# Performance work log

Hardware: AMD Instinct MI355X
Metric: run time of the kernel (lower is better)

Reference implementation:

```python
import jax, jax.numpy as jnp
import numpy as np

HIDDEN = 1024
HEADS = 16
HEAD_DIM = HIDDEN // HEADS


def rotate_half(x):
    x1, x2 = jnp.split(x, 2, axis=-1)
    return jnp.concatenate([-x2, x1], axis=-1)


def rope_cos_sin(T, head_dim):
    inv_freq = 1.0 / (10000.0 ** (jnp.arange(0, head_dim, 2, dtype=jnp.float32) / head_dim))
    pos = jnp.arange(T, dtype=jnp.float32)
    freqs = jnp.einsum('i,j->ij', pos, inv_freq)          # [T, head_dim/2]
    emb = jnp.concatenate([freqs, freqs], axis=-1)        # [T, head_dim]
    # broadcast shape [1, T, 1, head_dim]
    return jnp.cos(emb)[None, :, None, :], jnp.sin(emb)[None, :, None, :]


def setup_inputs() -> dict:
    key = jax.random.key(0)
    ks = jax.random.split(key, 9)
    B, T = 4, 2048
    s = 1.0 / np.sqrt(HIDDEN)
    x = jax.random.normal(ks[0], (B, T, HIDDEN), dtype=jnp.float32)
    Wq = jax.random.uniform(ks[1], (HIDDEN, HIDDEN), minval=-s, maxval=s, dtype=jnp.float32)
    bq = jax.random.uniform(ks[2], (HIDDEN,), minval=-s, maxval=s, dtype=jnp.float32)
    Wk = jax.random.uniform(ks[3], (HIDDEN, HIDDEN), minval=-s, maxval=s, dtype=jnp.float32)
    bk = jax.random.uniform(ks[4], (HIDDEN,), minval=-s, maxval=s, dtype=jnp.float32)
    Wv = jax.random.uniform(ks[5], (HIDDEN, HIDDEN), minval=-s, maxval=s, dtype=jnp.float32)
    bv = jax.random.uniform(ks[6], (HIDDEN,), minval=-s, maxval=s, dtype=jnp.float32)
    Wo = jax.random.uniform(ks[7], (HIDDEN, HIDDEN), minval=-s, maxval=s, dtype=jnp.float32)
    bo = jax.random.uniform(ks[8], (HIDDEN,), minval=-s, maxval=s, dtype=jnp.float32)
    return {"x": x, "Wq": Wq, "bq": bq, "Wk": Wk, "bk": bk,
            "Wv": Wv, "bv": bv, "Wo": Wo, "bo": bo}


def reference(x, Wq, bq, Wk, bk, Wv, bv, Wo, bo):
    B, T, _ = x.shape
    q = (x @ Wq + bq).reshape(B, T, HEADS, HEAD_DIM)
    k = (x @ Wk + bk).reshape(B, T, HEADS, HEAD_DIM)
    v = (x @ Wv + bv).reshape(B, T, HEADS, HEAD_DIM)
    cos, sin = rope_cos_sin(T, HEAD_DIM)
    q = q * cos + rotate_half(q) * sin
    k = k * cos + rotate_half(k) * sin
    scale = jnp.sqrt(jnp.float32(HEAD_DIM))
    scores = jnp.einsum('bqhd,bkhd->bhqk', q, k) / scale   # [B,H,T,T]
    causal = jnp.tril(jnp.ones((T, T), dtype=bool))
    scores = jnp.where(causal[None, None], scores, -jnp.inf)
    probs = jax.nn.softmax(scores, axis=-1)
    attn = jnp.einsum('bhqk,bkhd->bqhd', probs, v).reshape(B, T, HIDDEN)
    return attn @ Wo + bo
```

## Files before the change

### kernel.cpp

```cpp
#include <hip/hip_runtime.h>

typedef unsigned short u16;
typedef __attribute__((ext_vector_type(4))) float f32x4;
typedef __attribute__((ext_vector_type(16))) float f32x16;
typedef __attribute__((ext_vector_type(8))) short s16x8;

#define B_   4
#define T_   2048
#define H_   16
#define D_   64
#define HID  1024
#define BT   (B_*T_)
#define N3   3072

#define BARRIER() do { asm volatile("" ::: "memory"); __builtin_amdgcn_s_barrier(); asm volatile("" ::: "memory"); } while (0)

__device__ inline u16 f2b(float f) {
  union { float f; unsigned u; } v; v.f = f;
  unsigned u = v.u;
  unsigned r = (u + 0x7FFFu + ((u >> 16) & 1u)) >> 16;
  return (u16)r;
}

__device__ inline void gll16(const u16* g, u16* l) {
  __builtin_amdgcn_global_load_lds(
      (const __attribute__((address_space(1))) unsigned int*)g,
      (__attribute__((address_space(3))) unsigned int*)l, 16, 0, 0);
}

__device__ inline int swz8(int row) { return (row ^ (row >> 3)) & 7; }

__global__ void k_cast4(const float* __restrict__ src, u16* __restrict__ dst, int n4) {
  int i = blockIdx.x * blockDim.x + threadIdx.x;
  if (i >= n4) return;
  float4 v = ((const float4*)src)[i];
  ushort4 o;
  o.x = f2b(v.x); o.y = f2b(v.y); o.z = f2b(v.z); o.w = f2b(v.w);
  ((ushort4*)dst)[i] = o;
}

__global__ void k_ropetab(float2* __restrict__ tab) {
  int i = blockIdx.x * blockDim.x + threadIdx.x;
  int d = i & 31, t = i >> 5;
  float inv = expf(-0.28782313662425574f * (float)d);
  float ang = (float)t * inv;
  float c, s;
  sincosf(ang, &s, &c);
  tab[i] = make_float2(c, s);
}

__global__ __launch_bounds__(256) void k_packT(const float* __restrict__ W0,
                                               const float* __restrict__ W1,
                                               const float* __restrict__ W2,
                                               u16* __restrict__ Wt) {
  __shared__ float L[64][68];
  int n0 = blockIdx.x * 64, k0 = blockIdx.y * 64;
  int which = n0 >> 10;
  const float* W = (which == 0) ? W0 : (which == 1) ? W1 : W2;
  int nc = n0 & 1023;
  int tid = threadIdx.x;
  #pragma unroll
  for (int i = 0; i < 4; i++) {
    int ch = tid + 256 * i;
    int kr = ch >> 4, cc = ch & 15;
    float4 v = *(const float4*)(W + (size_t)(k0 + kr) * 1024 + nc + cc * 4);
    *(float4*)(&L[kr][cc * 4]) = v;
  }
  __syncthreads();
  #pragma unroll
  for (int i = 0; i < 2; i++) {
    int ch = tid + 256 * i;
    int nr = ch >> 3, ck = ch & 7;
    u16 tmp[8];
    #pragma unroll
    for (int j = 0; j < 8; j++) tmp[j] = f2b(L[ck * 8 + j][nr]);
    *(uint4*)(Wt + (size_t)(n0 + nr) * 1024 + k0 + ck * 8) = *(uint4*)tmp;
  }
}

__global__ __launch_bounds__(512) void gemm256(
    const u16* __restrict__ A, const u16* __restrict__ Bt,
    const float* __restrict__ b0, const float* __restrict__ b1,
    const float* __restrict__ b2, const float2* __restrict__ tab,
    u16* __restrict__ outp)
{
  __shared__ __align__(16) char SM[135168];
  const int tid = threadIdx.x, lane = tid & 63, w = tid >> 6;
  const int l15 = lane & 15, g = lane >> 4;
  const int wm = (w >> 2) * 128, wn = (w & 3) * 64;
  const int mbase = blockIdx.y * 256, nbase = blockIdx.x * 256;
  const int K = 1024, NT = 32;
  f32x4 acc[8][4] = {};

  auto SA = [&](int buf, int t) {
    u16* dst = (u16*)(SM + buf * 32768);
    #pragma unroll
    for (int i = 0; i < 2; i++) {
      int f = w * 128 + i * 64 + lane;
      int row = f >> 2, c = (f & 3) ^ (row & 3);
      gll16(A + (size_t)(mbase + row) * K + t * 32 + c * 8, dst + f * 8);
    }
  };
  auto SB = [&](int buf, int t) {
    u16* dst = (u16*)(SM + buf * 32768 + 16384);
    #pragma unroll
    for (int i = 0; i < 2; i++) {
      int f = w * 128 + i * 64 + lane;
      int row = f >> 2, c = (f & 3) ^ (row & 3);
      gll16(Bt + (size_t)(nbase + row) * K + t * 32 + c * 8, dst + f * 8);
    }
  };

  SA(0, 0); SB(0, 0); SA(1, 1); SB(1, 1);
  asm volatile("s_waitcnt vmcnt(4)" ::: "memory");
  BARRIER();

  int cur = 0;
  for (int t = 0; t < NT; t++) {
    int nx = cur + 2; if (nx >= 3) nx -= 3;
    const char* Ab = SM + cur * 32768;
    const char* Bb = SM + cur * 32768 + 16384;
    bool st = (t + 2 < NT);

    s16x8 af[8], bf[4];
    #pragma unroll
    for (int mt = 0; mt < 8; mt++) {
      int row = wm + mt * 16 + l15;
      af[mt] = *(const s16x8*)(Ab + row * 64 + (g ^ (row & 3)) * 16);
    }
    #pragma unroll
    for (int nt = 0; nt < 2; nt++) {
      int row = wn + nt * 16 + l15;
      bf[nt] = *(const s16x8*)(Bb + row * 64 + (g ^ (row & 3)) * 16);
    }
    if (st) SA(nx, t + 2);
    BARRIER();
    __builtin_amdgcn_s_setprio(1);
    #pragma unroll
    for (int mt = 0; mt < 8; mt++) {
      acc[mt][0] = __builtin_amdgcn_mfma_f32_16x16x32_bf16(af[mt], bf[0], acc[mt][0], 0, 0, 0);
      acc[mt][1] = __builtin_amdgcn_mfma_f32_16x16x32_bf16(af[mt], bf[1], acc[mt][1], 0, 0, 0);
    }
    __builtin_amdgcn_s_setprio(0);
    BARRIER();

    #pragma unroll
    for (int nt = 2; nt < 4; nt++) {
      int row = wn + nt * 16 + l15;
      bf[nt] = *(const s16x8*)(Bb + row * 64 + (g ^ (row & 3)) * 16);
    }
    if (st) SB(nx, t + 2);
    BARRIER();
    __builtin_amdgcn_s_setprio(1);
    #pragma unroll
    for (int mt = 0; mt < 8; mt++) {
      acc[mt][2] = __builtin_amdgcn_mfma_f32_16x16x32_bf16(af[mt], bf[2], acc[mt][2], 0, 0, 0);
      acc[mt][3] = __builtin_amdgcn_mfma_f32_16x16x32_bf16(af[mt], bf[3], acc[mt][3], 0, 0, 0);
    }
    __builtin_amdgcn_s_setprio(0);
    if (t + 1 < NT) {
      if (st) asm volatile("s_waitcnt vmcnt(4)" ::: "memory");
      else    asm volatile("s_waitcnt vmcnt(0)" ::: "memory");
    }
    BARRIER();
    cur = (cur == 2) ? 0 : cur + 1;
  }

  int which = nbase >> 10;
  const float* bp = (which == 0) ? b0 : (which == 1) ? b1 : b2;
  u16* Lt = (u16*)SM;
  if (which < 2) {
    const float FSC = (which == 0) ? 0.18033688011112043f : 1.0f;
    #pragma unroll
    for (int mt = 0; mt < 8; mt++) {
      #pragma unroll
      for (int r = 0; r < 4; r++) {
        int ml = wm + mt * 16 + g * 4 + r;
        int t = (mbase + ml) & (T_ - 1);
        #pragma unroll
        for (int nt = 0; nt < 2; nt++) {
          int d = nt * 16 + l15;
          float2 cs = tab[t * 32 + d];
          float a0 = acc[mt][nt][r]     + bp[(nbase + wn + d) & 1023];
          float a1 = acc[mt][nt + 2][r] + bp[(nbase + wn + d + 32) & 1023];
          Lt[ml * 264 + wn + d]      = f2b((a0 * cs.x - a1 * cs.y) * FSC);
          Lt[ml * 264 + wn + d + 32] = f2b((a1 * cs.x + a0 * cs.y) * FSC);
        }
      }
    }
    __syncthreads();
    #pragma unroll
    for (int i = 0; i < 16; i++) {
      int c = tid + 512 * i;
      int row = c >> 5, cc = c & 31;
      int gm = mbase + row, t = gm & (T_ - 1), bb = gm >> 11;
      int gn0 = nbase + cc * 8, h = (gn0 >> 6) & 15, d0 = gn0 & 63;
      *(uint4*)(outp + ((size_t)((which * B_ + bb) * H_ + h) * T_ + t) * D_ + d0) =
          *(const uint4*)(Lt + row * 264 + cc * 8);
    }
  } else {
    #pragma unroll
    for (int mt = 0; mt < 8; mt++) {
      #pragma unroll
      for (int nt = 0; nt < 4; nt++) {
        int nl = wn + nt * 16 + l15;
        float bias = bp[(nbase + nl) & 1023];
        u16 t4[4];
        #pragma unroll
        for (int r = 0; r < 4; r++) t4[r] = f2b(acc[mt][nt][r] + bias);
        *(uint2*)(Lt + nl * 264 + wm + mt * 16 + g * 4) = *(uint2*)t4;
      }
    }
    __syncthreads();
    #pragma unroll
    for (int i = 0; i < 16; i++) {
      int c = tid + 512 * i;
      int row = c >> 5, cc = c & 31;
      int gn = nbase + row, h = (gn >> 6) & 15, d = gn & 63;
      int m0 = mbase + cc * 8, bb = m0 >> 11, t0 = m0 & (T_ - 1);
      *(uint4*)(outp + ((size_t)((2 * B_ + bb) * H_ + h) * D_ + d) * T_ + t0) =
          *(const uint4*)(Lt + row * 264 + cc * 8);
    }
  }
}

template<int MODE>
__global__ __launch_bounds__(256) void gemm_k(
    const u16* __restrict__ A, const u16* __restrict__ Bt,
    const float* __restrict__ b0, void* __restrict__ outp, int N, int K)
{
  __shared__ __align__(16) u16 As[2][128 * 32];
  __shared__ __align__(16) u16 Bs[2][128 * 32];
  int tid = threadIdx.x, lane = tid & 63, w = tid >> 6;
  int l15 = lane & 15, g = lane >> 4;
  int wm = (w >> 1) * 64, wn = (w & 1) * 64;
  int mbase = blockIdx.y * 128, nbase = blockIdx.x * 128;
  f32x4 acc[4][4] = {};

  auto STAGE = [&](int bufi, int k0) {
    #pragma unroll
    for (int i = 0; i < 2; i++) {
      int f = i * 256 + tid;
      int row = f >> 2, c = f & 3;
      gll16(A  + (size_t)(mbase + row) * K + k0 + c * 8, &As[bufi][f * 8]);
      gll16(Bt + (size_t)(nbase + row) * K + k0 + c * 8, &Bs[bufi][f * 8]);
    }
  };

  STAGE(0, 0);
  int cur = 0;
  for (int k0 = 0; k0 < K; k0 += 32) {
    __syncthreads();
    if (k0 + 32 < K) STAGE(cur ^ 1, k0 + 32);
    s16x8 af[4], bf[4];
    #pragma unroll
    for (int mt = 0; mt < 4; mt++)
      af[mt] = *(const s16x8*)(&As[cur][(wm + mt * 16 + l15) * 32 + g * 8]);
    #pragma unroll
    for (int nt = 0; nt < 4; nt++)
      bf[nt] = *(const s16x8*)(&Bs[cur][(wn + nt * 16 + l15) * 32 + g * 8]);
    #pragma unroll
    for (int mt = 0; mt < 4; mt++)
      #pragma unroll
      for (int nt = 0; nt < 4; nt++)
        acc[mt][nt] = __builtin_amdgcn_mfma_f32_16x16x32_bf16(af[mt], bf[nt], acc[mt][nt], 0, 0, 0);
    cur ^= 1;
  }

  #pragma unroll
  for (int mt = 0; mt < 4; mt++)
    #pragma unroll
    for (int nt = 0; nt < 4; nt++)
      #pragma unroll
      for (int r = 0; r < 4; r++) {
        int gm = mbase + wm + mt * 16 + g * 4 + r;
        int gn = nbase + wn + nt * 16 + l15;
        ((float*)outp)[(size_t)gm * N + gn] = acc[mt][nt][r] + b0[gn];
      }
}

__global__ __launch_bounds__(512, 4) void k_flash(const u16* __restrict__ Qh,
                                                  const u16* __restrict__ Kh,
                                                  const u16* __restrict__ Vtg,
                                                  u16* __restrict__ O) {
  __shared__ __align__(16) char smem[65536];
  const int tid = threadIdx.x;
  const int lane = tid & 63;
  const int l31 = lane & 31, hi = lane >> 5;
  const int w = tid >> 6, grp = w >> 2, wi = w & 3;
  const int tidg = tid & 255;
  const int bh = blockIdx.x, p = blockIdx.y;
  const int b = bh >> 4, h = bh & 15;
  const size_t hb = (size_t)bh * T_ * D_;

  u16* kbase = (u16*)(smem + grp * 32768);

  const int f0 = tidg, f1 = 256 + tidg;
  const int r0 = f0 >> 3, c0 = (f0 & 7) ^ swz8(r0);
  const int r1 = f1 >> 3, c1 = (f1 & 7) ^ swz8(r1);
  const u16* kg0 = Kh + hb + (size_t)r0 * 64 + c0 * 8;
  const u16* kg1 = Kh + hb + (size_t)r1 * 64 + c1 * 8;
  const u16* vg0 = Vtg + hb + (size_t)r0 * T_ + c0 * 8;
  const u16* vg1 = Vtg + hb + (size_t)r1 * T_ + c1 * 8;

  auto STAGE = [&](int bufi, int kvblk) {
    u16* kb = kbase + bufi * 8192;
    int kv0 = kvblk * 64;
    gll16(kg0 + (size_t)kv0 * 64, kb + f0 * 8);
    gll16(kg1 + (size_t)kv0 * 64, kb + f1 * 8);
    gll16(vg0 + kv0, kb + 4096 + f0 * 8);
    gll16(vg1 + kv0, kb + 4096 + f1 * 8);
  };

  const int sw = (grp == 1) ? (2 * p + 2) : 17;
  int tile = (grp == 1) ? p : (15 - p);

  s16x8 qf[4];
  auto LOADQ = [&](int tl) {
    const u16* qp = Qh + hb + (size_t)(tl * 128 + wi * 32 + l31) * 64 + hi * 8;
    #pragma unroll
    for (int kc = 0; kc < 4; kc++) qf[kc] = *(const s16x8*)(qp + kc * 16);
  };
  LOADQ(tile);

  f32x16 o0 = {}, o1 = {};
  float l_ = 0.f;

  auto EPI = [&](int tl) {
    float inv = 1.0f / l_;
    int q = tl * 128 + wi * 32 + l31;
    size_t ob = ((size_t)b * T_ + q) * HID + h * 64 + hi * 4;
    #pragma unroll
    for (int k = 0; k < 4; k++) {
      u16 t4[4];
      #pragma unroll
      for (int j = 0; j < 4; j++) t4[j] = f2b(o0[k * 4 + j] * inv);
      *(uint2*)(O + ob + k * 8) = *(uint2*)t4;
      #pragma unroll
      for (int j = 0; j < 4; j++) t4[j] = f2b(o1[k * 4 + j] * inv);
      *(uint2*)(O + ob + 32 + k * 8) = *(uint2*)t4;
    }
  };

  STAGE(0, 0);
  for (int i = 0; i < 17; i++) {
    __syncthreads();
    if (i + 1 < 17) {
      int nb = (i + 1 < sw) ? (i + 1) : (17 + (i + 1) - sw);
      STAGE((i + 1) & 1, nb);
    }
    if (grp == 1 && i == sw) {
      EPI(tile);
      f32x16 z = {};
      o0 = z; o1 = z; l_ = 0.f;
      tile = 15 - p;
      LOADQ(tile);
    }
    int kvblk = (i < sw) ? i : (17 + i - sw);
    int kv0 = kvblk * 64;
    int qw0 = tile * 128 + wi * 32;
    if (kv0 > qw0 + 31) continue;

    const char* Kb = (const char*)kbase + (i & 1) * 16384;
    const char* Vb = Kb + 8192;

    f32x16 S0 = {}, S1 = {};
    const int swzl = swz8(l31) << 4, swzh = swz8(32 + l31) << 4;
    __builtin_amdgcn_s_setprio(1);
    #pragma unroll
    for (int kc = 0; kc < 4; kc++) {
      s16x8 kf0 = *(const s16x8*)(Kb + ((l31 * 128 + kc * 32 + hi * 16) ^ swzl));
      s16x8 kf1 = *(const s16x8*)(Kb + (((32 + l31) * 128 + kc * 32 + hi * 16) ^ swzh));
      S0 = __builtin_amdgcn_mfma_f32_32x32x16_bf16(kf0, qf[kc], S0, 0, 0, 0);
      S1 = __builtin_amdgcn_mfma_f32_32x32x16_bf16(kf1, qf[kc], S1, 0, 0, 0);
    }
    __builtin_amdgcn_s_setprio(0);

    if (kv0 + 63 > qw0) {
      int qrel = qw0 + l31 - kv0 - 4 * hi;
      #pragma unroll
      for (int r = 0; r < 16; r++) {
        const int kvr = (r & 3) + 8 * (r >> 2);
        if (kvr > qrel)      S0[r] = -__builtin_inff();
        if (kvr + 32 > qrel) S1[r] = -__builtin_inff();
      }
    }

    float rs = 0.f;
    __builtin_amdgcn_s_setprio(1);
    #pragma unroll
    for (int h2 = 0; h2 < 2; h2++) {
      #pragma unroll
      for (int cc = 0; cc < 2; cc++) {
        float e[8];
        #pragma unroll
        for (int j = 0; j < 8; j++) {
          int r = cc * 8 + j;
          e[j] = __builtin_exp2f(h2 ? S1[r] : S0[r]);
          rs += e[j];
        }
        unsigned p0, p1, p2, p3;
        asm("v_cvt_pk_bf16_f32 %0, %1, %2" : "=v"(p0) : "v"(e[0]), "v"(e[1]));
        asm("v_cvt_pk_bf16_f32 %0, %1, %2" : "=v"(p1) : "v"(e[2]), "v"(e[3]));
        asm("v_cvt_pk_bf16_f32 %0, %1, %2" : "=v"(p2) : "v"(e[4]), "v"(e[5]));
        asm("v_cvt_pk_bf16_f32 %0, %1, %2" : "=v"(p3) : "v"(e[6]), "v"(e[7]));
        asm("v_permlane32_swap_b32 %0, %1" : "+v"(p0), "+v"(p2));
        asm("v_permlane32_swap_b32 %0, %1" : "+v"(p1), "+v"(p3));
        union { unsigned u[4]; s16x8 v; } pb;
        pb.u[0] = p0; pb.u[1] = p1; pb.u[2] = p2; pb.u[3] = p3;
        const int kk = h2 * 2 + cc;
        s16x8 vf0 = *(const s16x8*)(Vb + ((l31 * 128 + kk * 32 + hi * 16) ^ swzl));
        s16x8 vf1 = *(const s16x8*)(Vb + (((32 + l31) * 128 + kk * 32 + hi * 16) ^ swzh));
        o0 = __builtin_amdgcn_mfma_f32_32x32x16_bf16(vf0, pb.v, o0, 0, 0, 0);
        o1 = __builtin_amdgcn_mfma_f32_32x32x16_bf16(vf1, pb.v, o1, 0, 0, 0);
      }
    }
    __builtin_amdgcn_s_setprio(0);
    rs += __shfl_xor(rs, 32);
    l_ += rs;
  }

  __syncthreads();
  float* mb = (float*)smem;
  if (grp == 1) {
    float* rrow = mb + (wi * 64 + lane) * 36;
    #pragma unroll
    for (int k = 0; k < 4; k++) {
      f32x4 v0, v1;
      #pragma unroll
      for (int j = 0; j < 4; j++) { v0[j] = o0[k * 4 + j]; v1[j] = o1[k * 4 + j]; }
      *(f32x4*)(rrow + k * 4) = v0;
      *(f32x4*)(rrow + 16 + k * 4) = v1;
    }
    rrow[32] = l_;
  }
  __syncthreads();
  if (grp == 0) {
    float* rrow = mb + (wi * 64 + lane) * 36;
    l_ += rrow[32];
    #pragma unroll
    for (int k = 0; k < 4; k++) {
      f32x4 v0 = *(const f32x4*)(rrow + k * 4);
      f32x4 v1 = *(const f32x4*)(rrow + 16 + k * 4);
      #pragma unroll
      for (int j = 0; j < 4; j++) {
        o0[k * 4 + j] += v0[j];
        o1[k * 4 + j] += v1[j];
      }
    }
    EPI(15 - p);
  }
}

extern "C" void kernel_launch(void* const* d_in, const int* in_sizes, int n_in,
                              void* d_out, int out_size, void* d_ws, size_t ws_size,
                              hipStream_t stream) {
  const float* x  = (const float*)d_in[0];
  const float* Wq = (const float*)d_in[1];
  const float* bq = (const float*)d_in[2];
  const float* Wk = (const float*)d_in[3];
  const float* bk = (const float*)d_in[4];
  const float* Wv = (const float*)d_in[5];
  const float* bv = (const float*)d_in[6];
  const float* Wo = (const float*)d_in[7];
  const float* bo = (const float*)d_in[8];
  float* out = (float*)d_out;

  char* ws = (char*)d_ws;
  u16* xb    = (u16*)(ws);
  u16* WqkvT = (u16*)(ws + (size_t)16777216);
  u16* WoT   = (u16*)(ws + (size_t)16777216 + 6291456);
  u16* QKVh  = (u16*)(ws + (size_t)16777216 + 6291456 + 2097152);
  u16* Oattn = xb;
  float2* tab = (float2*)WoT;

  k_cast4<<<(BT * HID / 4 + 255) / 256, 256, 0, stream>>>(x, xb, BT * HID / 4);
  k_packT<<<dim3(N3 / 64, HID / 64), 256, 0, stream>>>(Wq, Wk, Wv, WqkvT);
  k_ropetab<<<256, 256, 0, stream>>>(tab);

  gemm256<<<dim3(N3 / 256, BT / 256), 512, 0, stream>>>(
      xb, WqkvT, bq, bk, bv, tab, QKVh);

  k_packT<<<dim3(HID / 64, HID / 64), 256, 0, stream>>>(Wo, Wo, Wo, WoT);

  k_flash<<<dim3(B_ * H_, 8), 512, 0, stream>>>(
      QKVh, QKVh + (size_t)BT * HID, QKVh + 2 * (size_t)BT * HID, Oattn);

  gemm_k<1><<<dim3(HID / 128, BT / 128), 256, 0, stream>>>(
      Oattn, WoT, bo, (void*)out, HID, HID);
}
```

Baseline: 191.7 us.

## Deepen GEMM K-tile to 64 with staggered half-tile prefetch pipeline

The bf16 GEMM K-step grows from 32 to 64, so the loop runs 16 iterations instead of 32, with a wider 8-way XOR swizzle in LDS. Triple buffering is replaced by double buffering, where A half-tiles are prefetched one step ahead and B half-tiles two steps ahead. The prefetches are spread across four MFMA phases per iteration, each guarded by barriers. The aim is fewer barriers and waitcnts per unit of MFMA work and better overlap of loads with compute. The cost is more LDS per stage, more fragment registers, and a more intricate buffer-reuse schedule that depends on B fragments already sitting in registers before their buffer is overwritten.

```diff
diff --git a/kernel.cpp b/kernel.cpp
--- a/kernel.cpp
+++ b/kernel.cpp
@@ -78,7 +78,7 @@
   }
 }
 
-__global__ __launch_bounds__(512) void gemm256(
+__global__ __launch_bounds__(512, 2) void gemm256(
     const u16* __restrict__ A, const u16* __restrict__ Bt,
     const float* __restrict__ b0, const float* __restrict__ b1,
     const float* __restrict__ b2, const float2* __restrict__ tab,
@@ -89,86 +89,119 @@
   const int l15 = lane & 15, g = lane >> 4;
   const int wm = (w >> 2) * 128, wn = (w & 3) * 64;
   const int mbase = blockIdx.y * 256, nbase = blockIdx.x * 256;
-  const int K = 1024, NT = 32;
+  const int K = 1024, NT = 16;
   f32x4 acc[8][4] = {};
 
-  auto SA = [&](int buf, int t) {
-    u16* dst = (u16*)(SM + buf * 32768);
+  auto SHALF = [&](const u16* src, int base, int buf, int isB, int half, int t) {
+    u16* dst = (u16*)(SM + buf * 65536 + isB * 32768 + half * 16384);
     #pragma unroll
     for (int i = 0; i < 2; i++) {
-      int f = w * 128 + i * 64 + lane;
-      int row = f >> 2, c = (f & 3) ^ (row & 3);
-      gll16(A + (size_t)(mbase + row) * K + t * 32 + c * 8, dst + f * 8);
+      int f = i * 512 + tid;
+      int r = f >> 3, c = f & 7;
+      int row = half * 128 + r;
+      int cs = c ^ (row & 7);
+      gll16(src + (size_t)(base + row) * K + t * 64 + cs * 8, dst + f * 8);
     }
   };
-  auto SB = [&](int buf, int t) {
-    u16* dst = (u16*)(SM + buf * 32768 + 16384);
-    #pragma unroll
-    for (int i = 0; i < 2; i++) {
-      int f = w * 128 + i * 64 + lane;
-      int row = f >> 2, c = (f & 3) ^ (row & 3);
-      gll16(Bt + (size_t)(nbase + row) * K + t * 32 + c * 8, dst + f * 8);
-    }
+  auto RD = [&](const char* buf, int row, int kc) -> s16x8 {
+    int slot = (kc * 4 + g) ^ (row & 7);
+    return *(const s16x8*)(buf + row * 128 + slot * 16);
   };
 
-  SA(0, 0); SB(0, 0); SA(1, 1); SB(1, 1);
+  SHALF(A, mbase, 0, 0, 0, 0); SHALF(A, mbase, 0, 0, 1, 0);
+  SHALF(Bt, nbase, 0, 1, 0, 0); SHALF(Bt, nbase, 0, 1, 1, 0);
+  SHALF(Bt, nbase, 1, 1, 0, 1); SHALF(Bt, nbase, 1, 1, 1, 1);
   asm volatile("s_waitcnt vmcnt(4)" ::: "memory");
   BARRIER();
 
-  int cur = 0;
+  s16x8 af[4][2], bf[4][2];
   for (int t = 0; t < NT; t++) {
-    int nx = cur + 2; if (nx >= 3) nx -= 3;
-    const char* Ab = SM + cur * 32768;
-    const char* Bb = SM + cur * 32768 + 16384;
-    bool st = (t + 2 < NT);
-
-    s16x8 af[8], bf[4];
-    #pragma unroll
-    for (int mt = 0; mt < 8; mt++) {
-      int row = wm + mt * 16 + l15;
-      af[mt] = *(const s16x8*)(Ab + row * 64 + (g ^ (row & 3)) * 16);
+    const char* Ab = SM + (t & 1) * 65536;
+    const char* Bb = Ab + 32768;
+    const int nxA = (t + 1) & 1;
+    const int nxB = t & 1;
+
+    #pragma unroll
+    for (int mt = 0; mt < 4; mt++) {
+      af[mt][0] = RD(Ab, wm + mt * 16 + l15, 0);
+      af[mt][1] = RD(Ab, wm + mt * 16 + l15, 1);
     }
     #pragma unroll
     for (int nt = 0; nt < 2; nt++) {
-      int row = wn + nt * 16 + l15;
-      bf[nt] = *(const s16x8*)(Bb + row * 64 + (g ^ (row & 3)) * 16);
-    }
-    if (st) SA(nx, t + 2);
+      bf[nt][0] = RD(Bb, wn + nt * 16 + l15, 0);
+      bf[nt][1] = RD(Bb, wn + nt * 16 + l15, 1);
+    }
+    if (t + 1 < NT) SHALF(A, mbase, nxA, 0, 0, t + 1);
     BARRIER();
     __builtin_amdgcn_s_setprio(1);
     #pragma unroll
-    for (int mt = 0; mt < 8; mt++) {
-      acc[mt][0] = __builtin_amdgcn_mfma_f32_16x16x32_bf16(af[mt], bf[0], acc[mt][0], 0, 0, 0);
-      acc[mt][1] = __builtin_amdgcn_mfma_f32_16x16x32_bf16(af[mt], bf[1], acc[mt][1], 0, 0, 0);
-    }
+    for (int mt = 0; mt < 4; mt++)
+      #pragma unroll
+      for (int nt = 0; nt < 2; nt++) {
+        acc[mt][nt] = __builtin_amdgcn_mfma_f32_16x16x32_bf16(af[mt][0], bf[nt][0], acc[mt][nt], 0, 0, 0);
+        acc[mt][nt] = __builtin_amdgcn_mfma_f32_16x16x32_bf16(af[mt][1], bf[nt][1], acc[mt][nt], 0, 0, 0);
+      }
     __builtin_amdgcn_s_setprio(0);
     BARRIER();
 
     #pragma unroll
     for (int nt = 2; nt < 4; nt++) {
-      int row = wn + nt * 16 + l15;
-      bf[nt] = *(const s16x8*)(Bb + row * 64 + (g ^ (row & 3)) * 16);
-    }
-    if (st) SB(nx, t + 2);
+      bf[nt][0] = RD(Bb, wn + nt * 16 + l15, 0);
+      bf[nt][1] = RD(Bb, wn + nt * 16 + l15, 1);
+    }
+    if (t + 1 < NT) SHALF(A, mbase, nxA, 0, 1, t + 1);
     BARRIER();
     __builtin_amdgcn_s_setprio(1);
     #pragma unroll
-    for (int mt = 0; mt < 8; mt++) {
-      acc[mt][2] = __builtin_amdgcn_mfma_f32_16x16x32_bf16(af[mt], bf[2], acc[mt][2], 0, 0, 0);
-      acc[mt][3] = __builtin_amdgcn_mfma_f32_16x16x32_bf16(af[mt], bf[3], acc[mt][3], 0, 0, 0);
-    }
+    for (int mt = 0; mt < 4; mt++)
+      #pragma unroll
+      for (int nt = 2; nt < 4; nt++) {
+        acc[mt][nt] = __builtin_amdgcn_mfma_f32_16x16x32_bf16(af[mt][0], bf[nt][0], acc[mt][nt], 0, 0, 0);
+        acc[mt][nt] = __builtin_amdgcn_mfma_f32_16x16x32_bf16(af[mt][1], bf[nt][1], acc[mt][nt], 0, 0, 0);
+      }
+    __builtin_amdgcn_s_setprio(0);
+    BARRIER();
+
+    #pragma unroll
+    for (int mt = 0; mt < 4; mt++) {
+      af[mt][0] = RD(Ab, wm + (mt + 4) * 16 + l15, 0);
+      af[mt][1] = RD(Ab, wm + (mt + 4) * 16 + l15, 1);
+    }
+    if (t + 2 < NT) SHALF(Bt, nbase, nxB, 1, 0, t + 2);
+    BARRIER();
+    __builtin_amdgcn_s_setprio(1);
+    #pragma unroll
+    for (int mt = 0; mt < 4; mt++)
+      #pragma unroll
+      for (int nt = 0; nt < 2; nt++) {
+        acc[mt + 4][nt] = __builtin_amdgcn_mfma_f32_16x16x32_bf16(af[mt][0], bf[nt][0], acc[mt + 4][nt], 0, 0, 0);
+        acc[mt + 4][nt] = __builtin_amdgcn_mfma_f32_16x16x32_bf16(af[mt][1], bf[nt][1], acc[mt + 4][nt], 0, 0, 0);
+      }
+    __builtin_amdgcn_s_setprio(0);
+    BARRIER();
+
+    if (t + 2 < NT) SHALF(Bt, nbase, nxB, 1, 1, t + 2);
+    BARRIER();
+    __builtin_amdgcn_s_setprio(1);
+    #pragma unroll
+    for (int mt = 0; mt < 4; mt++)
+      #pragma unroll
+      for (int nt = 2; nt < 4; nt++) {
+        acc[mt + 4][nt] = __builtin_amdgcn_mfma_f32_16x16x32_bf16(af[mt][0], bf[nt][0], acc[mt + 4][nt], 0, 0, 0);
+        acc[mt + 4][nt] = __builtin_amdgcn_mfma_f32_16x16x32_bf16(af[mt][1], bf[nt][1], acc[mt + 4][nt], 0, 0, 0);
+      }
     __builtin_amdgcn_s_setprio(0);
     if (t + 1 < NT) {
-      if (st) asm volatile("s_waitcnt vmcnt(4)" ::: "memory");
-      else    asm volatile("s_waitcnt vmcnt(0)" ::: "memory");
-    }
-    BARRIER();
-    cur = (cur == 2) ? 0 : cur + 1;
+      if (t + 2 < NT) asm volatile("s_waitcnt vmcnt(4)" ::: "memory");
+      else            asm volatile("s_waitcnt vmcnt(0)" ::: "memory");
+    }
+    BARRIER();
   }
 
   int which = nbase >> 10;
   const float* bp = (which == 0) ? b0 : (which == 1) ? b1 : b2;
   u16* Lt = (u16*)SM;
+  BARRIER();
   if (which < 2) {
     const float FSC = (which == 0) ? 0.18033688011112043f : 1.0f;
     #pragma unroll
```

After: 185.9 us. 3.0% less time.

## Shrink QKV GEMM LDS to double buffer for two blocks per CU, swizzle block order

Applied to the files above, without the earlier changes.

Replaces the three-stage, split-phase pipelined QKV GEMM (with manual vmcnt waits and XOR-swizzled LDS) with a simple double-buffered loop. This halves shared memory so two 512-thread blocks can fit per CU, declared via launch_bounds(512,2). The epilogue now writes through LDS in two halves so it fits the smaller buffer. Both GEMM kernels also remap block indices with an XCD-aware swizzle to improve L2 locality. The trade-off is the loss of LDS bank-conflict swizzling and of the deeper prefetch, plus register pressure from the 2-block bound with 128 accumulator floats.

```diff
diff --git a/kernel.cpp b/kernel.cpp
--- a/kernel.cpp
+++ b/kernel.cpp
@@ -12,8 +12,6 @@
 #define HID  1024
 #define BT   (B_*T_)
 #define N3   3072
-
-#define BARRIER() do { asm volatile("" ::: "memory"); __builtin_amdgcn_s_barrier(); asm volatile("" ::: "memory"); } while (0)
 
 __device__ inline u16 f2b(float f) {
   union { float f; unsigned u; } v; v.f = f;
@@ -78,92 +76,54 @@
   }
 }
 
-__global__ __launch_bounds__(512) void gemm256(
+__global__ __launch_bounds__(512, 2) void gemm256(
     const u16* __restrict__ A, const u16* __restrict__ Bt,
     const float* __restrict__ b0, const float* __restrict__ b1,
     const float* __restrict__ b2, const float2* __restrict__ tab,
     u16* __restrict__ outp)
 {
-  __shared__ __align__(16) char SM[135168];
+  __shared__ __align__(16) char SM[67584];
+  u16* Ab = (u16*)SM;
+  u16* Bb = (u16*)(SM + 32768);
   const int tid = threadIdx.x, lane = tid & 63, w = tid >> 6;
   const int l15 = lane & 15, g = lane >> 4;
   const int wm = (w >> 2) * 128, wn = (w & 3) * 64;
-  const int mbase = blockIdx.y * 256, nbase = blockIdx.x * 256;
+  const int orig = blockIdx.y * 12 + blockIdx.x;
+  const int swzb = (orig & 7) * 48 + (orig >> 3);
+  const int mbase = (swzb / 12) * 256, nbase = (swzb % 12) * 256;
   const int K = 1024, NT = 32;
   f32x4 acc[8][4] = {};
 
-  auto SA = [&](int buf, int t) {
-    u16* dst = (u16*)(SM + buf * 32768);
+  auto STAGE = [&](int buf, int t) {
     #pragma unroll
     for (int i = 0; i < 2; i++) {
-      int f = w * 128 + i * 64 + lane;
-      int row = f >> 2, c = (f & 3) ^ (row & 3);
-      gll16(A + (size_t)(mbase + row) * K + t * 32 + c * 8, dst + f * 8);
+      int f = i * 512 + tid;
+      int r = f >> 2, c = f & 3;
+      gll16(A  + (size_t)(mbase + r) * K + t * 32 + c * 8, Ab + buf * 8192 + f * 8);
+      gll16(Bt + (size_t)(nbase + r) * K + t * 32 + c * 8, Bb + buf * 8192 + f * 8);
     }
   };
-  auto SB = [&](int buf, int t) {
-    u16* dst = (u16*)(SM + buf * 32768 + 16384);
-    #pragma unroll
-    for (int i = 0; i < 2; i++) {
-      int f = w * 128 + i * 64 + lane;
-      int row = f >> 2, c = (f & 3) ^ (row & 3);
-      gll16(Bt + (size_t)(nbase + row) * K + t * 32 + c * 8, dst + f * 8);
-    }
-  };
-
-  SA(0, 0); SB(0, 0); SA(1, 1); SB(1, 1);
-  asm volatile("s_waitcnt vmcnt(4)" ::: "memory");
-  BARRIER();
-
-  int cur = 0;
+
+  STAGE(0, 0);
   for (int t = 0; t < NT; t++) {
-    int nx = cur + 2; if (nx >= 3) nx -= 3;
-    const char* Ab = SM + cur * 32768;
-    const char* Bb = SM + cur * 32768 + 16384;
-    bool st = (t + 2 < NT);
-
+    __syncthreads();
+    if (t + 1 < NT) STAGE((t + 1) & 1, t + 1);
+    const u16* Ac = Ab + (t & 1) * 8192;
+    const u16* Bc = Bb + (t & 1) * 8192;
     s16x8 af[8], bf[4];
     #pragma unroll
-    for (int mt = 0; mt < 8; mt++) {
-      int row = wm + mt * 16 + l15;
-      af[mt] = *(const s16x8*)(Ab + row * 64 + (g ^ (row & 3)) * 16);
-    }
-    #pragma unroll
-    for (int nt = 0; nt < 2; nt++) {
-      int row = wn + nt * 16 + l15;
-      bf[nt] = *(const s16x8*)(Bb + row * 64 + (g ^ (row & 3)) * 16);
-    }
-    if (st) SA(nx, t + 2);
-    BARRIER();
+    for (int mt = 0; mt < 8; mt++)
+      af[mt] = *(const s16x8*)(Ac + (wm + mt * 16 + l15) * 32 + g * 8);
+    #pragma unroll
+    for (int nt = 0; nt < 4; nt++)
+      bf[nt] = *(const s16x8*)(Bc + (wn + nt * 16 + l15) * 32 + g * 8);
     __builtin_amdgcn_s_setprio(1);
     #pragma unroll
-    for (int mt = 0; mt < 8; mt++) {
-      acc[mt][0] = __builtin_amdgcn_mfma_f32_16x16x32_bf16(af[mt], bf[0], acc[mt][0], 0, 0, 0);
-      acc[mt][1] = __builtin_amdgcn_mfma_f32_16x16x32_bf16(af[mt], bf[1], acc[mt][1], 0, 0, 0);
-    }
+    for (int mt = 0; mt < 8; mt++)
+      #pragma unroll
+      for (int nt = 0; nt < 4; nt++)
+        acc[mt][nt] = __builtin_amdgcn_mfma_f32_16x16x32_bf16(af[mt], bf[nt], acc[mt][nt], 0, 0, 0);
     __builtin_amdgcn_s_setprio(0);
-    BARRIER();
-
-    #pragma unroll
-    for (int nt = 2; nt < 4; nt++) {
-      int row = wn + nt * 16 + l15;
-      bf[nt] = *(const s16x8*)(Bb + row * 64 + (g ^ (row & 3)) * 16);
-    }
-    if (st) SB(nx, t + 2);
-    BARRIER();
-    __builtin_amdgcn_s_setprio(1);
-    #pragma unroll
-    for (int mt = 0; mt < 8; mt++) {
-      acc[mt][2] = __builtin_amdgcn_mfma_f32_16x16x32_bf16(af[mt], bf[2], acc[mt][2], 0, 0, 0);
-      acc[mt][3] = __builtin_amdgcn_mfma_f32_16x16x32_bf16(af[mt], bf[3], acc[mt][3], 0, 0, 0);
-    }
-    __builtin_amdgcn_s_setprio(0);
-    if (t + 1 < NT) {
-      if (st) asm volatile("s_waitcnt vmcnt(4)" ::: "memory");
-      else    asm volatile("s_waitcnt vmcnt(0)" ::: "memory");
-    }
-    BARRIER();
-    cur = (cur == 2) ? 0 : cur + 1;
   }
 
   int which = nbase >> 10;
@@ -172,54 +132,66 @@
   if (which < 2) {
     const float FSC = (which == 0) ? 0.18033688011112043f : 1.0f;
     #pragma unroll
-    for (int mt = 0; mt < 8; mt++) {
-      #pragma unroll
-      for (int r = 0; r < 4; r++) {
-        int ml = wm + mt * 16 + g * 4 + r;
-        int t = (mbase + ml) & (T_ - 1);
+    for (int hf = 0; hf < 2; hf++) {
+      __syncthreads();
+      if ((w >> 2) == hf) {
         #pragma unroll
-        for (int nt = 0; nt < 2; nt++) {
-          int d = nt * 16 + l15;
-          float2 cs = tab[t * 32 + d];
-          float a0 = acc[mt][nt][r]     + bp[(nbase + wn + d) & 1023];
-          float a1 = acc[mt][nt + 2][r] + bp[(nbase + wn + d + 32) & 1023];
-          Lt[ml * 264 + wn + d]      = f2b((a0 * cs.x - a1 * cs.y) * FSC);
-          Lt[ml * 264 + wn + d + 32] = f2b((a1 * cs.x + a0 * cs.y) * FSC);
+        for (int mt = 0; mt < 8; mt++) {
+          #pragma unroll
+          for (int r = 0; r < 4; r++) {
+            int ml = mt * 16 + g * 4 + r;
+            int t = (mbase + hf * 128 + ml) & (T_ - 1);
+            #pragma unroll
+            for (int nt = 0; nt < 2; nt++) {
+              int d = nt * 16 + l15;
+              float2 cs = tab[t * 32 + d];
+              float a0 = acc[mt][nt][r]     + bp[(nbase + wn + d) & 1023];
+              float a1 = acc[mt][nt + 2][r] + bp[(nbase + wn + d + 32) & 1023];
+              Lt[ml * 264 + wn + d]      = f2b((a0 * cs.x - a1 * cs.y) * FSC);
+              Lt[ml * 264 + wn + d + 32] = f2b((a1 * cs.x + a0 * cs.y) * FSC);
+            }
+          }
         }
       }
-    }
-    __syncthreads();
-    #pragma unroll
-    for (int i = 0; i < 16; i++) {
-      int c = tid + 512 * i;
-      int row = c >> 5, cc = c & 31;
-      int gm = mbase + row, t = gm & (T_ - 1), bb = gm >> 11;
-      int gn0 = nbase + cc * 8, h = (gn0 >> 6) & 15, d0 = gn0 & 63;
-      *(uint4*)(outp + ((size_t)((which * B_ + bb) * H_ + h) * T_ + t) * D_ + d0) =
-          *(const uint4*)(Lt + row * 264 + cc * 8);
+      __syncthreads();
+      #pragma unroll
+      for (int i = 0; i < 8; i++) {
+        int c = tid + 512 * i;
+        int row = c >> 5, cc = c & 31;
+        int gm = mbase + hf * 128 + row, t = gm & (T_ - 1), bb = gm >> 11;
+        int gn0 = nbase + cc * 8, h = (gn0 >> 6) & 15, d0 = gn0 & 63;
+        *(uint4*)(outp + ((size_t)((which * B_ + bb) * H_ + h) * T_ + t) * D_ + d0) =
+            *(const uint4*)(Lt + row * 264 + cc * 8);
+      }
     }
   } else {
     #pragma unroll
-    for (int mt = 0; mt < 8; mt++) {
-      #pragma unroll
-      for (int nt = 0; nt < 4; nt++) {
-        int nl = wn + nt * 16 + l15;
-        float bias = bp[(nbase + nl) & 1023];
-        u16 t4[4];
+    for (int hf = 0; hf < 2; hf++) {
+      __syncthreads();
+      if (((w & 3) >> 1) == hf) {
         #pragma unroll
-        for (int r = 0; r < 4; r++) t4[r] = f2b(acc[mt][nt][r] + bias);
-        *(uint2*)(Lt + nl * 264 + wm + mt * 16 + g * 4) = *(uint2*)t4;
-      }
-    }
-    __syncthreads();
-    #pragma unroll
-    for (int i = 0; i < 16; i++) {
-      int c = tid + 512 * i;
-      int row = c >> 5, cc = c & 31;
-      int gn = nbase + row, h = (gn >> 6) & 15, d = gn & 63;
-      int m0 = mbase + cc * 8, bb = m0 >> 11, t0 = m0 & (T_ - 1);
-      *(uint4*)(outp + ((size_t)((2 * B_ + bb) * H_ + h) * D_ + d) * T_ + t0) =
-          *(const uint4*)(Lt + row * 264 + cc * 8);
+        for (int mt = 0; mt < 8; mt++) {
+          #pragma unroll
+          for (int nt = 0; nt < 4; nt++) {
+            int nl = ((w & 3) & 1) * 64 + nt * 16 + l15;
+            float bias = bp[(nbase + hf * 128 + nl) & 1023];
+            u16 t4[4];
+            #pragma unroll
+            for (int r = 0; r < 4; r++) t4[r] = f2b(acc[mt][nt][r] + bias);
+            *(uint2*)(Lt + nl * 264 + wm + mt * 16 + g * 4) = *(uint2*)t4;
+          }
+        }
+      }
+      __syncthreads();
+      #pragma unroll
+      for (int i = 0; i < 8; i++) {
+        int c = tid + 512 * i;
+        int row = c >> 5, cc = c & 31;
+        int gn = nbase + hf * 128 + row, h = (gn >> 6) & 15, d = gn & 63;
+        int m0 = mbase + cc * 8, bb = m0 >> 11, t0 = m0 & (T_ - 1);
+        *(uint4*)(outp + ((size_t)((2 * B_ + bb) * H_ + h) * D_ + d) * T_ + t0) =
+            *(const uint4*)(Lt + row * 264 + cc * 8);
+      }
     }
   }
 }
@@ -234,7 +206,9 @@
   int tid = threadIdx.x, lane = tid & 63, w = tid >> 6;
   int l15 = lane & 15, g = lane >> 4;
   int wm = (w >> 1) * 64, wn = (w & 1) * 64;
-  int mbase = blockIdx.y * 128, nbase = blockIdx.x * 128;
+  int orig = blockIdx.y * 8 + blockIdx.x;
+  int swzb = (orig & 7) * 64 + (orig >> 3);
+  int mbase = (swzb >> 3) * 128, nbase = (swzb & 7) * 128;
   f32x4 acc[4][4] = {};
 
   auto STAGE = [&](int bufi, int k0) {
```

Result: no change. 190.0 us (-0.9%).
